# Performance work log

Measured on AMD Instinct MI355X. Metric: run time of the kernel, lower is better.

Reference implementation:

```python
import jax, jax.numpy as jnp
import numpy as np

N, E, IN, OUT = 50000, 800000, 128, 128
R = 5  # num_rels + 1 (last slice is the self-loop weight)


def setup_inputs() -> dict:
    key = jax.random.key(0)
    k = jax.random.split(key, 6)
    x = jax.random.normal(k[0], (N, IN), jnp.float32)
    src = jax.random.randint(k[1], (E,), 0, N)
    dst = jax.random.randint(k[2], (E,), 0, N)
    rel = jax.random.randint(k[3], (E,), 0, R - 1)  # edge rel_type in [0, num_rels)
    xavier = np.sqrt(2.0) * np.sqrt(6.0 / (IN + OUT))  # gain('relu') * xavier bound scale
    weight = jax.random.uniform(k[4], (R, IN, OUT), jnp.float32, -xavier, xavier)
    bias = jax.random.uniform(k[5], (R, OUT), jnp.float32, -xavier, xavier)
    return dict(x=x, weight=weight, bias=bias, src=src, dst=dst, rel=rel)


def reference(x, weight, bias, src, dst, rel):
    num_nodes = x.shape[0]
    num_edge_rels = weight.shape[0] - 1
    x_src = x[src]  # [E, IN] per-edge source gather
    # Per-edge message: x_src @ weight[rel] + bias[rel].
    # Grouped-GEMM style: one dense GEMM per relation, select by mask
    # (avoids materializing [E, IN, OUT] per-edge weights).
    msg = jnp.zeros((src.shape[0], weight.shape[2]), x.dtype)
    for r in range(num_edge_rels):
        hr = x_src @ weight[r] + bias[r]  # [E, OUT]
        msg = jnp.where((rel == r)[:, None], hr, msg)
    # Max-aggregation onto destination nodes; DGL fills 0 for nodes w/o in-edges.
    agg = jax.ops.segment_max(msg, dst, num_segments=num_nodes)  # [N, OUT]
    deg = jax.ops.segment_sum(jnp.ones_like(dst, jnp.float32), dst, num_segments=num_nodes)
    agg = jnp.where((deg > 0)[:, None], agg, jnp.zeros((), x.dtype))
    # Self-loop transform with last weight/bias slice.
    h = x @ weight[-1] + bias[-1] + agg
    return h
```

## Files before the change

### kernel.cpp

```cpp
#include <hip/hip_runtime.h>

#define NNODES 50000
#define NEDGES 800000
#define DIM    128
#define NRELS  4
#define NBLK2  25
#define DBLK   128
#define NDB    (5*DBLK)
#define NFB    3125

typedef __attribute__((ext_vector_type(8))) short bf16x8;
typedef __attribute__((ext_vector_type(8))) unsigned short u16x8;
typedef __attribute__((ext_vector_type(4))) float f32x4;

#define SSRC_OFF 0
#define CNT_OFF  3200000
#define BSUM_OFF 3404800
#define RANK_OFF 3405056
#define WT_OFF   5005056
#define XBF_OFF  5168896
#define H_OFF    17968896

__device__ __forceinline__ unsigned short f2bf(float f) {
  unsigned u = __float_as_uint(f);
  return (unsigned short)((u + 0x7FFFu + ((u >> 16) & 1u)) >> 16);
}

__global__ void k_prep(const float* __restrict__ x, unsigned short* __restrict__ xbf,
                       const float* __restrict__ W, unsigned short* __restrict__ Wt,
                       const int* __restrict__ dst, unsigned* __restrict__ cnt,
                       unsigned short* __restrict__ rank) {
  int i = blockIdx.x * blockDim.x + threadIdx.x;
  if (i < NNODES * DIM / 8) {
    const float4* p = (const float4*)x + i * 2;
    float4 v0 = p[0], v1 = p[1];
    u16x8 o;
    o[0] = f2bf(v0.x); o[1] = f2bf(v0.y); o[2] = f2bf(v0.z); o[3] = f2bf(v0.w);
    o[4] = f2bf(v1.x); o[5] = f2bf(v1.y); o[6] = f2bf(v1.z); o[7] = f2bf(v1.w);
    *(u16x8*)(xbf + i * 8) = o;
  }
  if (i < 5 * DIM * DIM) {
    int r = i >> 14, rem = i & 16383, k = rem >> 7, c = rem & 127;
    Wt[(r << 14) + (c << 7) + k] = f2bf(W[i]);
  }
  if (i < NEDGES) {
    unsigned rk = atomicAdd(&cnt[dst[i]], 1u);
    rank[i] = (unsigned short)rk;
  }
}

__global__ void k_scanA(unsigned* __restrict__ cnt, unsigned* __restrict__ bsum) {
  __shared__ unsigned sh[256];
  int tid = threadIdx.x;
  int base = blockIdx.x * 2048 + tid * 8;
  unsigned v[8], tsum = 0;
#pragma unroll
  for (int j = 0; j < 8; j++) { v[j] = cnt[base + j]; tsum += v[j]; }
  sh[tid] = tsum;
  __syncthreads();
  for (int off = 1; off < 256; off <<= 1) {
    unsigned t = (tid >= off) ? sh[tid - off] : 0u;
    __syncthreads();
    sh[tid] += t;
    __syncthreads();
  }
  unsigned run = sh[tid] - tsum;
#pragma unroll
  for (int j = 0; j < 8; j++) { unsigned t = v[j]; cnt[base + j] = run; run += t; }
  if (tid == 255) bsum[blockIdx.x] = sh[255];
}

__global__ void k_fix(unsigned* __restrict__ cnt, const unsigned* __restrict__ bsum) {
  int blk = blockIdx.x;
  if (blk == 0) return;
  unsigned p = 0;
  for (int k = 0; k < blk; k++) p += bsum[k];
  int base = blk * 2048 + threadIdx.x * 8;
#pragma unroll
  for (int j = 0; j < 8; j++) cnt[base + j] += p;
}

__global__ __launch_bounds__(256, 2) void k_dfill(
    const unsigned short* __restrict__ xbf, const unsigned short* __restrict__ Wt,
    const float* __restrict__ bias, unsigned short* __restrict__ H,
    float* __restrict__ out, const int* __restrict__ rel, const int* __restrict__ dst,
    const int* __restrict__ src, const unsigned* __restrict__ cnt,
    const unsigned short* __restrict__ rank, unsigned* __restrict__ ssrc) {
  if (blockIdx.x >= NDB) {
    int e = (blockIdx.x - NDB) * 256 + threadIdx.x;
    if (e < NEDGES) {
      int r = rel[e]; r = r < 0 ? 0 : (r > NRELS - 1 ? NRELS - 1 : r);
      int d = dst[e];
      unsigned pos = cnt[d] + (unsigned)rank[e];
      ssrc[pos] = (unsigned)(r * NNODES + src[e]);
    }
    return;
  }
  __shared__ unsigned short st[4][2048];
  int lane = threadIdx.x & 63;
  int wv = threadIdx.x >> 6;
  int r = blockIdx.x / DBLK;
  const int NT = NNODES / 16;
  int col = lane & 15, quad = lane >> 4;

  const unsigned short* wr = Wt + (r << 14);
  bf16x8 B[8][4];
  float bs[8];
#pragma unroll
  for (int ct = 0; ct < 8; ct++) {
#pragma unroll
    for (int kk = 0; kk < 4; kk++)
      B[ct][kk] = *(const bf16x8*)(wr + ((ct * 16 + col) << 7) + kk * 32 + quad * 8);
    bs[ct] = bias[(r << 7) + ct * 16 + col];
  }

  for (int t = (blockIdx.x % DBLK) * 4 + wv; t < NT; t += DBLK * 4) {
    int n0 = t * 16;
    int na = n0 + col;
    bf16x8 a0 = *(const bf16x8*)(xbf + (na << 7) + quad * 8);
    bf16x8 a1 = *(const bf16x8*)(xbf + (na << 7) + 32 + quad * 8);
    bf16x8 a2 = *(const bf16x8*)(xbf + (na << 7) + 64 + quad * 8);
    bf16x8 a3 = *(const bf16x8*)(xbf + (na << 7) + 96 + quad * 8);

    if (r < NRELS) {
#pragma unroll
      for (int ct = 0; ct < 8; ct++) {
        f32x4 acc = {0.f, 0.f, 0.f, 0.f};
        acc = __builtin_amdgcn_mfma_f32_16x16x32_bf16(a0, B[ct][0], acc, 0, 0, 0);
        acc = __builtin_amdgcn_mfma_f32_16x16x32_bf16(a1, B[ct][1], acc, 0, 0, 0);
        acc = __builtin_amdgcn_mfma_f32_16x16x32_bf16(a2, B[ct][2], acc, 0, 0, 0);
        acc = __builtin_amdgcn_mfma_f32_16x16x32_bf16(a3, B[ct][3], acc, 0, 0, 0);
        int cc = ct * 16 + col;
#pragma unroll
        for (int j = 0; j < 4; j++) st[wv][(quad * 4 + j) * 128 + cc] = f2bf(acc[j] + bs[ct]);
      }
      unsigned short* gb = H + (((size_t)(r * NNODES + n0)) << 7);
#pragma unroll
      for (int s = 0; s < 4; s++) {
        int off = s * 512 + lane * 8;
        *(u16x8*)(gb + off) = *(const u16x8*)(&st[wv][off]);
      }
    } else {
#pragma unroll
      for (int ct = 0; ct < 8; ct++) {
        f32x4 acc = {0.f, 0.f, 0.f, 0.f};
        acc = __builtin_amdgcn_mfma_f32_16x16x32_bf16(a0, B[ct][0], acc, 0, 0, 0);
        acc = __builtin_amdgcn_mfma_f32_16x16x32_bf16(a1, B[ct][1], acc, 0, 0, 0);
        acc = __builtin_amdgcn_mfma_f32_16x16x32_bf16(a2, B[ct][2], acc, 0, 0, 0);
        acc = __builtin_amdgcn_mfma_f32_16x16x32_bf16(a3, B[ct][3], acc, 0, 0, 0);
        int cc = ct * 16 + col;
#pragma unroll
        for (int j = 0; j < 4; j++)
          out[((size_t)(n0 + quad * 4 + j) << 7) + (unsigned)cc] = acc[j] + bs[ct];
      }
    }
  }
}

__global__ __launch_bounds__(256, 4) void k_agg(
    const unsigned* __restrict__ cnt, const unsigned* __restrict__ ssrc,
    const uint2* __restrict__ H2, float* __restrict__ out) {
  int lane = threadIdx.x & 31;
  int half = threadIdx.x >> 5;
  int n = blockIdx.x * 8 + half;
  if (n >= NNODES) return;
  unsigned base = cnt[n];
  int deg = (int)(cnt[n + 1] - base);

  float m0 = -3.0e38f, m1 = -3.0e38f, m2 = -3.0e38f, m3 = -3.0e38f;
  int i = 0;
  for (; i + 4 <= deg; i += 4) {
    unsigned c0 = ssrc[base + i], c1 = ssrc[base + i + 1];
    unsigned c2 = ssrc[base + i + 2], c3 = ssrc[base + i + 3];
    uint2 v0 = H2[((size_t)c0 << 5) + lane];
    uint2 v1 = H2[((size_t)c1 << 5) + lane];
    uint2 v2 = H2[((size_t)c2 << 5) + lane];
    uint2 v3 = H2[((size_t)c3 << 5) + lane];
    m0 = fmaxf(m0, __uint_as_float(v0.x << 16));
    m1 = fmaxf(m1, __uint_as_float(v0.x & 0xFFFF0000u));
    m2 = fmaxf(m2, __uint_as_float(v0.y << 16));
    m3 = fmaxf(m3, __uint_as_float(v0.y & 0xFFFF0000u));
    m0 = fmaxf(m0, __uint_as_float(v1.x << 16));
    m1 = fmaxf(m1, __uint_as_float(v1.x & 0xFFFF0000u));
    m2 = fmaxf(m2, __uint_as_float(v1.y << 16));
    m3 = fmaxf(m3, __uint_as_float(v1.y & 0xFFFF0000u));
    m0 = fmaxf(m0, __uint_as_float(v2.x << 16));
    m1 = fmaxf(m1, __uint_as_float(v2.x & 0xFFFF0000u));
    m2 = fmaxf(m2, __uint_as_float(v2.y << 16));
    m3 = fmaxf(m3, __uint_as_float(v2.y & 0xFFFF0000u));
    m0 = fmaxf(m0, __uint_as_float(v3.x << 16));
    m1 = fmaxf(m1, __uint_as_float(v3.x & 0xFFFF0000u));
    m2 = fmaxf(m2, __uint_as_float(v3.y << 16));
    m3 = fmaxf(m3, __uint_as_float(v3.y & 0xFFFF0000u));
  }
  for (; i < deg; i++) {
    unsigned c = ssrc[base + i];
    uint2 v = H2[((size_t)c << 5) + lane];
    m0 = fmaxf(m0, __uint_as_float(v.x << 16));
    m1 = fmaxf(m1, __uint_as_float(v.x & 0xFFFF0000u));
    m2 = fmaxf(m2, __uint_as_float(v.y << 16));
    m3 = fmaxf(m3, __uint_as_float(v.y & 0xFFFF0000u));
  }
  float4* op = (float4*)(out + ((size_t)n << 7)) + lane;
  float4 s = *op;
  if (deg > 0) { s.x += m0; s.y += m1; s.z += m2; s.w += m3; }
  *op = s;
}

extern "C" void kernel_launch(void* const* d_in, const int* in_sizes, int n_in,
                              void* d_out, int out_size, void* d_ws, size_t ws_size,
                              hipStream_t stream) {
  const float* x = (const float*)d_in[0];
  const float* W = (const float*)d_in[1];
  const float* bias = (const float*)d_in[2];
  const int* src = (const int*)d_in[3];
  const int* dst = (const int*)d_in[4];
  const int* rel = (const int*)d_in[5];

  char* ws = (char*)d_ws;
  unsigned* ssrc = (unsigned*)(ws + SSRC_OFF);
  unsigned* cnt = (unsigned*)(ws + CNT_OFF);
  unsigned* bsum = (unsigned*)(ws + BSUM_OFF);
  unsigned short* rank = (unsigned short*)(ws + RANK_OFF);
  unsigned short* Wt = (unsigned short*)(ws + WT_OFF);
  unsigned short* xbf = (unsigned short*)(ws + XBF_OFF);
  unsigned short* H = (unsigned short*)(ws + H_OFF);
  float* out = (float*)d_out;

  hipMemsetAsync(cnt, 0, BSUM_OFF - CNT_OFF, stream);
  hipLaunchKernelGGL(k_prep, dim3(3125), dim3(256), 0, stream, x, xbf, W, Wt, dst, cnt, rank);
  hipLaunchKernelGGL(k_scanA, dim3(NBLK2), dim3(256), 0, stream, cnt, bsum);
  hipLaunchKernelGGL(k_fix, dim3(NBLK2), dim3(256), 0, stream, cnt, bsum);
  hipLaunchKernelGGL(k_dfill, dim3(NDB + NFB), dim3(256), 0, stream, xbf, Wt, bias, H, out, rel,
                     dst, src, cnt, rank, ssrc);
  hipLaunchKernelGGL(k_agg, dim3(6250), dim3(256), 0, stream, cnt, ssrc, (const uint2*)H, out);
}
```

Measured before the change: 204.5 us.

## Replace global-atomic degree counting with chunked LDS histograms and two-level scan

Destination-degree counting moves out of global atomics in the prep kernel into a new histogram kernel. Each block counts one edge chunk over half the node range using packed 16-bit counters in shared memory. A scan kernel then walks the per-chunk partial counts to build per-chunk prefix offsets and the node totals, and the fill stage adds the chunk prefix to each edge's position. This removes contention on global atomics and the memset, at the cost of an extra 6.4MB partial-count buffer that is read and written several times, plus a serial 64-step loop in a 25-block scan.

```diff
diff --git a/kernel.cpp b/kernel.cpp
--- a/kernel.cpp
+++ b/kernel.cpp
@@ -8,6 +8,9 @@
 #define DBLK   128
 #define NDB    (5*DBLK)
 #define NFB    3125
+#define EPB    12500
+#define NHC    64
+#define RNG    25000
 
 typedef __attribute__((ext_vector_type(8))) short bf16x8;
 typedef __attribute__((ext_vector_type(8))) unsigned short u16x8;
@@ -17,9 +20,10 @@
 #define CNT_OFF  3200000
 #define BSUM_OFF 3404800
 #define RANK_OFF 3405056
-#define WT_OFF   5005056
-#define XBF_OFF  5168896
-#define H_OFF    17968896
+#define PCNT_OFF 5005056
+#define WT_OFF   11405056
+#define XBF_OFF  11568896
+#define H_OFF    24368896
 
 __device__ __forceinline__ unsigned short f2bf(float f) {
   unsigned u = __float_as_uint(f);
@@ -27,9 +31,7 @@
 }
 
 __global__ void k_prep(const float* __restrict__ x, unsigned short* __restrict__ xbf,
-                       const float* __restrict__ W, unsigned short* __restrict__ Wt,
-                       const int* __restrict__ dst, unsigned* __restrict__ cnt,
-                       unsigned short* __restrict__ rank) {
+                       const float* __restrict__ W, unsigned short* __restrict__ Wt) {
   int i = blockIdx.x * blockDim.x + threadIdx.x;
   if (i < NNODES * DIM / 8) {
     const float4* p = (const float4*)x + i * 2;
@@ -43,19 +45,48 @@
     int r = i >> 14, rem = i & 16383, k = rem >> 7, c = rem & 127;
     Wt[(r << 14) + (c << 7) + k] = f2bf(W[i]);
   }
-  if (i < NEDGES) {
-    unsigned rk = atomicAdd(&cnt[dst[i]], 1u);
-    rank[i] = (unsigned short)rk;
-  }
-}
-
-__global__ void k_scanA(unsigned* __restrict__ cnt, unsigned* __restrict__ bsum) {
+}
+
+__global__ __launch_bounds__(1024) void k_hist(const int* __restrict__ dst,
+                                               unsigned short* __restrict__ rank,
+                                               unsigned short* __restrict__ pcnt) {
+  __shared__ unsigned lh[RNG / 2];
+  int c = blockIdx.x >> 1;
+  int r0 = (blockIdx.x & 1) * RNG;
+  for (int i = threadIdx.x; i < RNG / 2; i += 1024) lh[i] = 0u;
+  __syncthreads();
+  int e0 = c * EPB;
+  for (int e = e0 + threadIdx.x; e < e0 + EPB; e += 1024) {
+    int d = dst[e] - r0;
+    if ((unsigned)d < (unsigned)RNG) {
+      unsigned old = atomicAdd(&lh[d >> 1], (d & 1) ? 65536u : 1u);
+      rank[e] = (unsigned short)((old >> ((d & 1) << 4)) & 0xFFFFu);
+    }
+  }
+  __syncthreads();
+  unsigned* prow = (unsigned*)(pcnt + (size_t)c * NNODES + r0);
+  for (int i = threadIdx.x; i < RNG / 2; i += 1024) prow[i] = lh[i];
+}
+
+__global__ void k_scanB(unsigned short* __restrict__ pcnt, unsigned* __restrict__ cnt,
+                        unsigned* __restrict__ bsum) {
   __shared__ unsigned sh[256];
   int tid = threadIdx.x;
-  int base = blockIdx.x * 2048 + tid * 8;
-  unsigned v[8], tsum = 0;
-#pragma unroll
-  for (int j = 0; j < 8; j++) { v[j] = cnt[base + j]; tsum += v[j]; }
+  int bin0 = blockIdx.x * 2048 + tid * 8;
+  unsigned run[8] = {0, 0, 0, 0, 0, 0, 0, 0};
+  if (bin0 < NNODES) {
+    for (int b = 0; b < NHC; b++) {
+      size_t off = (size_t)b * NNODES + bin0;
+      u16x8 v = *(const u16x8*)(pcnt + off);
+      u16x8 w;
+#pragma unroll
+      for (int j = 0; j < 8; j++) { w[j] = (unsigned short)run[j]; run[j] += v[j]; }
+      *(u16x8*)(pcnt + off) = w;
+    }
+  }
+  unsigned tsum = 0;
+#pragma unroll
+  for (int j = 0; j < 8; j++) tsum += run[j];
   sh[tid] = tsum;
   __syncthreads();
   for (int off = 1; off < 256; off <<= 1) {
@@ -64,9 +95,9 @@
     sh[tid] += t;
     __syncthreads();
   }
-  unsigned run = sh[tid] - tsum;
-#pragma unroll
-  for (int j = 0; j < 8; j++) { unsigned t = v[j]; cnt[base + j] = run; run += t; }
+  unsigned r = sh[tid] - tsum;
+#pragma unroll
+  for (int j = 0; j < 8; j++) { unsigned t = run[j]; cnt[bin0 + j] = r; r += t; }
   if (tid == 255) bsum[blockIdx.x] = sh[255];
 }
 
@@ -85,13 +116,14 @@
     const float* __restrict__ bias, unsigned short* __restrict__ H,
     float* __restrict__ out, const int* __restrict__ rel, const int* __restrict__ dst,
     const int* __restrict__ src, const unsigned* __restrict__ cnt,
-    const unsigned short* __restrict__ rank, unsigned* __restrict__ ssrc) {
+    const unsigned short* __restrict__ rank, const unsigned short* __restrict__ pfx,
+    unsigned* __restrict__ ssrc) {
   if (blockIdx.x >= NDB) {
     int e = (blockIdx.x - NDB) * 256 + threadIdx.x;
     if (e < NEDGES) {
       int r = rel[e]; r = r < 0 ? 0 : (r > NRELS - 1 ? NRELS - 1 : r);
       int d = dst[e];
-      unsigned pos = cnt[d] + (unsigned)rank[e];
+      unsigned pos = cnt[d] + (unsigned)pfx[(size_t)(e / EPB) * NNODES + d] + (unsigned)rank[e];
       ssrc[pos] = (unsigned)(r * NNODES + src[e]);
     }
     return;
@@ -222,16 +254,17 @@
   unsigned* cnt = (unsigned*)(ws + CNT_OFF);
   unsigned* bsum = (unsigned*)(ws + BSUM_OFF);
   unsigned short* rank = (unsigned short*)(ws + RANK_OFF);
+  unsigned short* pcnt = (unsigned short*)(ws + PCNT_OFF);
   unsigned short* Wt = (unsigned short*)(ws + WT_OFF);
   unsigned short* xbf = (unsigned short*)(ws + XBF_OFF);
   unsigned short* H = (unsigned short*)(ws + H_OFF);
   float* out = (float*)d_out;
 
-  hipMemsetAsync(cnt, 0, BSUM_OFF - CNT_OFF, stream);
-  hipLaunchKernelGGL(k_prep, dim3(3125), dim3(256), 0, stream, x, xbf, W, Wt, dst, cnt, rank);
-  hipLaunchKernelGGL(k_scanA, dim3(NBLK2), dim3(256), 0, stream, cnt, bsum);
+  hipLaunchKernelGGL(k_prep, dim3(3125), dim3(256), 0, stream, x, xbf, W, Wt);
+  hipLaunchKernelGGL(k_hist, dim3(NHC * 2), dim3(1024), 0, stream, dst, rank, pcnt);
+  hipLaunchKernelGGL(k_scanB, dim3(NBLK2), dim3(256), 0, stream, pcnt, cnt, bsum);
   hipLaunchKernelGGL(k_fix, dim3(NBLK2), dim3(256), 0, stream, cnt, bsum);
   hipLaunchKernelGGL(k_dfill, dim3(NDB + NFB), dim3(256), 0, stream, xbf, Wt, bias, H, out, rel,
-                     dst, src, cnt, rank, ssrc);
+                     dst, src, cnt, rank, pcnt, ssrc);
   hipLaunchKernelGGL(k_agg, dim3(6250), dim3(256), 0, stream, cnt, ssrc, (const uint2*)H, out);
 }
```

Result: faster. 188.9 us (-7.6%).
